# Optimization experiments

Hardware: AMD Instinct MI355X
Metric: run time of the kernel (lower is better)

Reference implementation:

```python
import jax, jax.numpy as jnp
import numpy as np

N_NODES = 100000
N_EDGES = 1600000
IN_F = 256
OUT_F = 128


def setup_inputs() -> dict:
    key = jax.random.key(0)
    k1, k2, k3, k4, k5, k6 = jax.random.split(key, 6)
    x = jax.random.normal(k1, (N_NODES, IN_F), dtype=jnp.float32)
    edge_src = jax.random.randint(k2, (N_EDGES,), 0, N_NODES, dtype=jnp.int64)
    edge_dst = jax.random.randint(k3, (N_EDGES,), 0, N_NODES, dtype=jnp.int64)
    edge_weight = jax.random.uniform(k4, (N_EDGES,), dtype=jnp.float32)
    stdv = 1.0 / np.sqrt(OUT_F)
    w = jax.random.uniform(k5, (IN_F, OUT_F), dtype=jnp.float32, minval=-stdv, maxval=stdv)
    b = jax.random.uniform(k6, (OUT_F,), dtype=jnp.float32, minval=-stdv, maxval=stdv)
    return {"x": x, "edge_src": edge_src, "edge_dst": edge_dst,
            "edge_weight": edge_weight, "w": w, "b": b}


def reference(x, edge_src, edge_dst, edge_weight, w, b):
    # dense feature transform: [N, in] @ [in, out] -> [N, out]
    h = x @ w
    # sparse adjacency SpMM: out[i] = sum_{e: dst[e]==i} a[e] * h[src[e]]
    msgs = h[edge_src] * edge_weight[:, None]          # [E, out]
    agg = jax.ops.segment_sum(msgs, edge_dst, num_segments=N_NODES)
    return agg + b
```

## Files before the change

### kernel.cpp

```cpp
#include <hip/hip_runtime.h>

#define N_NODES 100000
#define N_EDGES 1600000
#define IN_F 256
#define OUT_F 128

#define NBUCK 1563
#define NCH   250
#define CH    6400
#define LSUB  8
#define LIST_CAP (LSUB * 256)

typedef __attribute__((ext_vector_type(8))) short bf16x8;
typedef __attribute__((ext_vector_type(4))) float f32x4;

static __device__ __forceinline__ unsigned f2bf_u(float f) {
    unsigned u = __float_as_uint(f);
    return (u + 0x7FFFu + ((u >> 16) & 1u)) >> 16;
}
static __device__ __forceinline__ float bf2f(short s) {
    return __uint_as_float(((unsigned)(unsigned short)s) << 16);
}

__global__ __launch_bounds__(256) void hist_kernel(const int* __restrict__ edge_dst,
                                                   int* __restrict__ hist) {
    __shared__ int h[NBUCK];
    const int t = threadIdx.x;
    for (int b = t; b < NBUCK; b += 256) h[b] = 0;
    __syncthreads();
    const int e0 = blockIdx.x * CH;
    #pragma unroll
    for (int i = 0; i < CH / 256; ++i)
        atomicAdd(&h[edge_dst[e0 + i * 256 + t] >> 6], 1);
    __syncthreads();
    int* o = hist + (size_t)blockIdx.x * NBUCK;
    for (int b = t; b < NBUCK; b += 256) o[b] = h[b];
}

__global__ __launch_bounds__(256) void scan1_kernel(int* __restrict__ hist,
                                                    int* __restrict__ btot) {
    const int b = blockIdx.x * 256 + threadIdx.x;
    if (b >= NBUCK) return;
    int run = 0;
    #pragma unroll 10
    for (int c = 0; c < NCH; ++c) {
        const size_t idx = (size_t)c * NBUCK + b;
        const int v = hist[idx];
        hist[idx] = run;
        run += v;
    }
    btot[b] = run;
}

__global__ __launch_bounds__(256) void scan2_kernel(const int* __restrict__ btot,
                                                    int* __restrict__ bstart) {
    __shared__ int wsum[4];
    const int t = threadIdx.x;
    const int lane = t & 63, wave = t >> 6;
    int v[7];
    int s = 0;
    #pragma unroll
    for (int j = 0; j < 7; ++j) {
        const int i = t * 7 + j;
        v[j] = (i < NBUCK) ? btot[i] : 0;
        s += v[j];
    }
    int sc = s;
    #pragma unroll
    for (int off = 1; off < 64; off <<= 1) {
        const int o = __shfl_up(sc, off);
        if (lane >= off) sc += o;
    }
    if (lane == 63) wsum[wave] = sc;
    __syncthreads();
    int add = 0;
    for (int w2 = 0; w2 < wave; ++w2) add += wsum[w2];
    int excl = add + sc - s;
    #pragma unroll
    for (int j = 0; j < 7; ++j) {
        const int i = t * 7 + j;
        if (i < NBUCK) bstart[i] = excl;
        excl += v[j];
    }
    if (t == 255) bstart[NBUCK] = add + sc;
}

__global__ __launch_bounds__(256) void scatter_kernel(const int* __restrict__ edge_src,
                                                      const int* __restrict__ edge_dst,
                                                      const float* __restrict__ edge_weight,
                                                      const int* __restrict__ hist,
                                                      const int* __restrict__ bstart,
                                                      int2* __restrict__ part) {
    __shared__ int cur[NBUCK];
    const int t = threadIdx.x;
    const int c = blockIdx.x;
    const int* hc = hist + (size_t)c * NBUCK;
    for (int b = t; b < NBUCK; b += 256) cur[b] = bstart[b] + hc[b];
    __syncthreads();
    const int e0 = c * CH;
    #pragma unroll
    for (int i = 0; i < CH / 256; ++i) {
        const int e = e0 + i * 256 + t;
        const int d = edge_dst[e];
        const int pos = atomicAdd(&cur[d >> 6], 1);
        part[pos] = make_int2(edge_src[e] | ((d & 63) << 24), __float_as_int(edge_weight[e]));
    }
}

__global__ __launch_bounds__(256) void wprep_kernel(const float* __restrict__ w,
                                                    unsigned short* __restrict__ wtf) {
    int id = blockIdx.x * 256 + threadIdx.x;
    if (id >= 4096) return;
    int f = id >> 6, lane = id & 63;
    int ks = f >> 3, nt = f & 7;
    int m = lane & 15, q = lane >> 4;
    int row = nt * 16 + m;
    int col0 = ks * 32 + q * 8;
    unsigned short* o = wtf + (size_t)f * 512 + lane * 8;
    #pragma unroll
    for (int j = 0; j < 8; ++j)
        o[j] = (unsigned short)f2bf_u(w[(size_t)(col0 + j) * OUT_F + row]);
}

__global__ __launch_bounds__(256) void gemm_mfma_kernel(const float* __restrict__ x,
                                                        const unsigned short* __restrict__ wtf,
                                                        unsigned short* __restrict__ hb) {
    __shared__ unsigned short xs[64][264];
    const int t = threadIdx.x;
    const int row0 = blockIdx.x * 64;

    const float4* x4 = (const float4*)x;
    #pragma unroll
    for (int i = 0; i < 16; ++i) {
        int idx = t + i * 256;
        int r = idx >> 6, c4 = idx & 63;
        int rg = row0 + r; if (rg >= N_NODES) rg = N_NODES - 1;
        float4 v = x4[(size_t)rg * 64 + c4];
        unsigned u0 = f2bf_u(v.x) | (f2bf_u(v.y) << 16);
        unsigned u1 = f2bf_u(v.z) | (f2bf_u(v.w) << 16);
        *(uint2*)&xs[r][c4 * 4] = make_uint2(u0, u1);
    }
    __syncthreads();

    const int wave = t >> 6, lane = t & 63;
    const int m = lane & 15, quad = lane >> 4;

    bf16x8 af[8];
    #pragma unroll
    for (int ks = 0; ks < 8; ++ks)
        af[ks] = *(const bf16x8*)&xs[wave * 16 + m][ks * 32 + quad * 8];

    f32x4 acc[8];
    #pragma unroll
    for (int nt = 0; nt < 8; ++nt) acc[nt] = (f32x4){0.f, 0.f, 0.f, 0.f};

    const bf16x8* wf = (const bf16x8*)wtf;
    #pragma unroll
    for (int ks = 0; ks < 8; ++ks) {
        #pragma unroll
        for (int nt = 0; nt < 8; ++nt) {
            bf16x8 bf = wf[(size_t)(ks * 8 + nt) * 64 + lane];
            acc[nt] = __builtin_amdgcn_mfma_f32_16x16x32_bf16(af[ks], bf, acc[nt], 0, 0, 0);
        }
    }

    const int tile_base = row0 + wave * 16;
    #pragma unroll
    for (int nt = 0; nt < 8; ++nt) {
        #pragma unroll
        for (int r = 0; r < 4; ++r) {
            int orow = tile_base + quad * 4 + r;
            if (orow < N_NODES)
                hb[(size_t)orow * OUT_F + nt * 16 + m] = (unsigned short)f2bf_u(acc[nt][r]);
        }
    }
}

__global__ __launch_bounds__(256) void spmm_kernel(const unsigned short* __restrict__ hb,
                                                   const int* __restrict__ bstart,
                                                   const int2* __restrict__ part,
                                                   const float* __restrict__ b,
                                                   float* __restrict__ out) {
    __shared__ int lh[64];
    __shared__ int lstart[65];
    __shared__ int lcur[64];
    __shared__ int2 list[LIST_CAP];

    const int t = threadIdx.x;
    const int base = blockIdx.x * 64;

    const int s0 = bstart[blockIdx.x];
    int cntb = bstart[blockIdx.x + 1] - s0;
    if (cntb > LIST_CAP) cntb = LIST_CAP;

    if (t < 64) lh[t] = 0;
    __syncthreads();

    int2 stash[LSUB];
    int  sn[LSUB];
    #pragma unroll
    for (int sub = 0; sub < LSUB; ++sub) {
        const int idx = sub * 256 + t;
        sn[sub] = -1;
        if (idx < cntb) {
            int2 en = part[(size_t)s0 + idx];
            int n = ((unsigned)en.x) >> 24;
            stash[sub] = make_int2(en.x & 0xFFFFFF, en.y);
            sn[sub] = n;
            atomicAdd(&lh[n], 1);
        }
    }
    __syncthreads();

    if (t < 64) {
        int v = lh[t];
        int s = v;
        #pragma unroll
        for (int off = 1; off < 64; off <<= 1) {
            int o = __shfl_up(s, off);
            if (t >= off) s += o;
        }
        lstart[t] = s - v;
        lcur[t]   = s - v;
        if (t == 63) lstart[64] = s;
    }
    __syncthreads();

    #pragma unroll
    for (int sub = 0; sub < LSUB; ++sub) {
        if (sn[sub] >= 0) {
            int pos = atomicAdd(&lcur[sn[sub]], 1);
            list[pos] = stash[sub];
        }
    }
    __syncthreads();

    const int j = t & 15;
    const float4* b4 = (const float4*)b;
    const float4 bb0 = b4[j * 2];
    const float4 bb1 = b4[j * 2 + 1];

    #pragma unroll
    for (int g = 0; g < 4; ++g) {
        const int n = g * 16 + (t >> 4);
        const int node = base + n;
        if (node >= N_NODES) continue;
        float4 acc0 = bb0, acc1 = bb1;
        const int p1 = lstart[n + 1];
        for (int p = lstart[n]; p < p1; ++p) {
            const int2 sw = list[p];
            const float wgt = __int_as_float(sw.y);
            const bf16x8 hv = *(const bf16x8*)(hb + (size_t)sw.x * OUT_F + j * 8);
            acc0.x += wgt * bf2f(hv[0]);
            acc0.y += wgt * bf2f(hv[1]);
            acc0.z += wgt * bf2f(hv[2]);
            acc0.w += wgt * bf2f(hv[3]);
            acc1.x += wgt * bf2f(hv[4]);
            acc1.y += wgt * bf2f(hv[5]);
            acc1.z += wgt * bf2f(hv[6]);
            acc1.w += wgt * bf2f(hv[7]);
        }
        float4* o4 = (float4*)(out + (size_t)node * OUT_F + j * 8);
        o4[0] = acc0;
        o4[1] = acc1;
    }
}

extern "C" void kernel_launch(void* const* d_in, const int* in_sizes, int n_in,
                              void* d_out, int out_size, void* d_ws, size_t ws_size,
                              hipStream_t stream) {
    const float* x           = (const float*)d_in[0];
    const int*   edge_src    = (const int*)d_in[1];
    const int*   edge_dst    = (const int*)d_in[2];
    const float* edge_weight = (const float*)d_in[3];
    const float* w           = (const float*)d_in[4];
    const float* b           = (const float*)d_in[5];
    float* out = (float*)d_out;

    char* ws = (char*)d_ws;
    size_t off = 0;
    unsigned short* hb  = (unsigned short*)(ws + off);
    off += (size_t)N_NODES * OUT_F * 2;           off = (off + 15) & ~(size_t)15;
    unsigned short* wtf = (unsigned short*)(ws + off);
    off += (size_t)IN_F * OUT_F * 2;              off = (off + 15) & ~(size_t)15;
    int* hist = (int*)(ws + off);
    off += (size_t)NCH * NBUCK * 4;               off = (off + 15) & ~(size_t)15;
    int* btot = (int*)(ws + off);
    off += (size_t)NBUCK * 4;                     off = (off + 15) & ~(size_t)15;
    int* bstart = (int*)(ws + off);
    off += (size_t)(NBUCK + 1) * 4;               off = (off + 15) & ~(size_t)15;
    int2* part = (int2*)(ws + off);
    off += (size_t)N_EDGES * 8;

    hist_kernel <<<NCH, 256, 0, stream>>>(edge_dst, hist);
    scan1_kernel<<<(NBUCK + 255) / 256, 256, 0, stream>>>(hist, btot);
    scan2_kernel<<<1, 256, 0, stream>>>(btot, bstart);
    scatter_kernel<<<NCH, 256, 0, stream>>>(edge_src, edge_dst, edge_weight, hist, bstart, part);
    wprep_kernel<<<16, 256, 0, stream>>>(w, wtf);
    gemm_mfma_kernel<<<(N_NODES + 63) / 64, 256, 0, stream>>>(x, wtf, hb);
    spmm_kernel<<<NBUCK, 256, 0, stream>>>(hb, bstart, part, b, out);
}
```

Measured before the change: 319.7 us.

## Fuse partition kernels into one cooperative kernel and split SpMM buckets in half

Merges the histogram, two scans, scatter and weight-prep kernels into a single cooperative kernel that uses grid-wide syncs and keeps edge data in registers between phases, so edges are read once and four launches go away. The SpMM kernel now launches two blocks per bucket, each handling 32 nodes, for more parallelism. Its gather loop is unrolled by four to keep more loads in flight. Trade-offs: grid syncs add latency, every SpMM block reads the whole bucket's edge list twice, and the list is capped at 1024 entries, which could drop edges on skewed inputs.

```diff
diff --git a/kernel.cpp b/kernel.cpp
--- a/kernel.cpp
+++ b/kernel.cpp
@@ -1,4 +1,7 @@
 #include <hip/hip_runtime.h>
+#include <hip/hip_cooperative_groups.h>
+
+namespace cg = cooperative_groups;
 
 #define N_NODES 100000
 #define N_EDGES 1600000
@@ -8,8 +11,9 @@
 #define NBUCK 1563
 #define NCH   250
 #define CH    6400
-#define LSUB  8
-#define LIST_CAP (LSUB * 256)
+#define CBT   1024
+#define EPT   7
+#define LIST_CAP 1024
 
 typedef __attribute__((ext_vector_type(8))) short bf16x8;
 typedef __attribute__((ext_vector_type(4))) float f32x4;
@@ -22,104 +26,112 @@
     return __uint_as_float(((unsigned)(unsigned short)s) << 16);
 }
 
-__global__ __launch_bounds__(256) void hist_kernel(const int* __restrict__ edge_dst,
-                                                   int* __restrict__ hist) {
+__global__ __launch_bounds__(CBT) void part_coop_kernel(
+    const int* __restrict__ edge_src, const int* __restrict__ edge_dst,
+    const float* __restrict__ edge_weight, const float* __restrict__ w,
+    int* __restrict__ hist, int* __restrict__ btot, int* __restrict__ bstart,
+    int2* __restrict__ part, unsigned short* __restrict__ wtf) {
+    cg::grid_group grid = cg::this_grid();
     __shared__ int h[NBUCK];
-    const int t = threadIdx.x;
-    for (int b = t; b < NBUCK; b += 256) h[b] = 0;
-    __syncthreads();
-    const int e0 = blockIdx.x * CH;
-    #pragma unroll
-    for (int i = 0; i < CH / 256; ++i)
-        atomicAdd(&h[edge_dst[e0 + i * 256 + t] >> 6], 1);
-    __syncthreads();
-    int* o = hist + (size_t)blockIdx.x * NBUCK;
-    for (int b = t; b < NBUCK; b += 256) o[b] = h[b];
-}
-
-__global__ __launch_bounds__(256) void scan1_kernel(int* __restrict__ hist,
-                                                    int* __restrict__ btot) {
-    const int b = blockIdx.x * 256 + threadIdx.x;
-    if (b >= NBUCK) return;
-    int run = 0;
-    #pragma unroll 10
-    for (int c = 0; c < NCH; ++c) {
-        const size_t idx = (size_t)c * NBUCK + b;
-        const int v = hist[idx];
-        hist[idx] = run;
-        run += v;
-    }
-    btot[b] = run;
-}
-
-__global__ __launch_bounds__(256) void scan2_kernel(const int* __restrict__ btot,
-                                                    int* __restrict__ bstart) {
-    __shared__ int wsum[4];
-    const int t = threadIdx.x;
-    const int lane = t & 63, wave = t >> 6;
-    int v[7];
-    int s = 0;
-    #pragma unroll
-    for (int j = 0; j < 7; ++j) {
-        const int i = t * 7 + j;
-        v[j] = (i < NBUCK) ? btot[i] : 0;
-        s += v[j];
-    }
-    int sc = s;
-    #pragma unroll
-    for (int off = 1; off < 64; off <<= 1) {
-        const int o = __shfl_up(sc, off);
-        if (lane >= off) sc += o;
-    }
-    if (lane == 63) wsum[wave] = sc;
-    __syncthreads();
-    int add = 0;
-    for (int w2 = 0; w2 < wave; ++w2) add += wsum[w2];
-    int excl = add + sc - s;
-    #pragma unroll
-    for (int j = 0; j < 7; ++j) {
-        const int i = t * 7 + j;
-        if (i < NBUCK) bstart[i] = excl;
-        excl += v[j];
-    }
-    if (t == 255) bstart[NBUCK] = add + sc;
-}
-
-__global__ __launch_bounds__(256) void scatter_kernel(const int* __restrict__ edge_src,
-                                                      const int* __restrict__ edge_dst,
-                                                      const float* __restrict__ edge_weight,
-                                                      const int* __restrict__ hist,
-                                                      const int* __restrict__ bstart,
-                                                      int2* __restrict__ part) {
-    __shared__ int cur[NBUCK];
+    __shared__ int wsum[CBT / 64];
+
     const int t = threadIdx.x;
     const int c = blockIdx.x;
-    const int* hc = hist + (size_t)c * NBUCK;
-    for (int b = t; b < NBUCK; b += 256) cur[b] = bstart[b] + hc[b];
-    __syncthreads();
     const int e0 = c * CH;
-    #pragma unroll
-    for (int i = 0; i < CH / 256; ++i) {
-        const int e = e0 + i * 256 + t;
-        const int d = edge_dst[e];
-        const int pos = atomicAdd(&cur[d >> 6], 1);
-        part[pos] = make_int2(edge_src[e] | ((d & 63) << 24), __float_as_int(edge_weight[e]));
-    }
-}
-
-__global__ __launch_bounds__(256) void wprep_kernel(const float* __restrict__ w,
-                                                    unsigned short* __restrict__ wtf) {
-    int id = blockIdx.x * 256 + threadIdx.x;
-    if (id >= 4096) return;
-    int f = id >> 6, lane = id & 63;
-    int ks = f >> 3, nt = f & 7;
-    int m = lane & 15, q = lane >> 4;
-    int row = nt * 16 + m;
-    int col0 = ks * 32 + q * 8;
-    unsigned short* o = wtf + (size_t)f * 512 + lane * 8;
-    #pragma unroll
-    for (int j = 0; j < 8; ++j)
-        o[j] = (unsigned short)f2bf_u(w[(size_t)(col0 + j) * OUT_F + row]);
+
+    for (int i = t; i < NBUCK; i += CBT) h[i] = 0;
+    __syncthreads();
+    int dv[EPT], sv[EPT], wv[EPT];
+    #pragma unroll
+    for (int i = 0; i < EPT; ++i) {
+        const int k = i * CBT + t;
+        dv[i] = -1;
+        if (k < CH) {
+            const int e = e0 + k;
+            dv[i] = edge_dst[e];
+            sv[i] = edge_src[e];
+            wv[i] = __float_as_int(edge_weight[e]);
+            atomicAdd(&h[dv[i] >> 6], 1);
+        }
+    }
+    __syncthreads();
+    {
+        int* o = hist + (size_t)c * NBUCK;
+        for (int i = t; i < NBUCK; i += CBT) o[i] = h[i];
+    }
+    __threadfence();
+    grid.sync();
+
+    const int gt = c * CBT + t;
+    if (gt < NBUCK) {
+        int run = 0;
+        #pragma unroll 10
+        for (int ch = 0; ch < NCH; ++ch) {
+            const size_t idx = (size_t)ch * NBUCK + gt;
+            const int v = hist[idx];
+            hist[idx] = run;
+            run += v;
+        }
+        btot[gt] = run;
+    } else if (c >= 16 && c < 20) {
+        const int id = (c - 16) * CBT + t;
+        const int f = id >> 6, lane = id & 63;
+        const int ks = f >> 3, nt = f & 7;
+        const int m = lane & 15, q = lane >> 4;
+        const int row = nt * 16 + m;
+        const int col0 = ks * 32 + q * 8;
+        unsigned short* o = wtf + (size_t)f * 512 + lane * 8;
+        #pragma unroll
+        for (int jj = 0; jj < 8; ++jj)
+            o[jj] = (unsigned short)f2bf_u(w[(size_t)(col0 + jj) * OUT_F + row]);
+    }
+    __threadfence();
+    grid.sync();
+
+    if (c == 0) {
+        const int lane = t & 63, wave = t >> 6;
+        int v[2];
+        int s = 0;
+        #pragma unroll
+        for (int jj = 0; jj < 2; ++jj) {
+            const int i = t * 2 + jj;
+            v[jj] = (i < NBUCK) ? btot[i] : 0;
+            s += v[jj];
+        }
+        int sc = s;
+        #pragma unroll
+        for (int off = 1; off < 64; off <<= 1) {
+            const int o = __shfl_up(sc, off);
+            if (lane >= off) sc += o;
+        }
+        if (lane == 63) wsum[wave] = sc;
+        __syncthreads();
+        int add = 0;
+        for (int w2 = 0; w2 < wave; ++w2) add += wsum[w2];
+        int excl = add + sc - s;
+        #pragma unroll
+        for (int jj = 0; jj < 2; ++jj) {
+            const int i = t * 2 + jj;
+            if (i < NBUCK) bstart[i] = excl;
+            excl += v[jj];
+        }
+        if (t == CBT - 1) bstart[NBUCK] = add + sc;
+        __threadfence();
+    }
+    grid.sync();
+
+    {
+        const int* hc = hist + (size_t)c * NBUCK;
+        for (int i = t; i < NBUCK; i += CBT) h[i] = bstart[i] + hc[i];
+    }
+    __syncthreads();
+    #pragma unroll
+    for (int i = 0; i < EPT; ++i) {
+        if (dv[i] >= 0) {
+            const int pos = atomicAdd(&h[dv[i] >> 6], 1);
+            part[pos] = make_int2(sv[i] | ((dv[i] & 63) << 24), wv[i]);
+        }
+    }
 }
 
 __global__ __launch_bounds__(256) void gemm_mfma_kernel(const float* __restrict__ x,
@@ -181,56 +193,61 @@
                                                    const int2* __restrict__ part,
                                                    const float* __restrict__ b,
                                                    float* __restrict__ out) {
-    __shared__ int lh[64];
-    __shared__ int lstart[65];
-    __shared__ int lcur[64];
+    __shared__ int lh[32];
+    __shared__ int lstart[33];
+    __shared__ int lcur[32];
     __shared__ int2 list[LIST_CAP];
 
     const int t = threadIdx.x;
-    const int base = blockIdx.x * 64;
-
-    const int s0 = bstart[blockIdx.x];
-    int cntb = bstart[blockIdx.x + 1] - s0;
-    if (cntb > LIST_CAP) cntb = LIST_CAP;
-
-    if (t < 64) lh[t] = 0;
-    __syncthreads();
-
-    int2 stash[LSUB];
-    int  sn[LSUB];
-    #pragma unroll
-    for (int sub = 0; sub < LSUB; ++sub) {
+    const int bucket = blockIdx.x >> 1;
+    const int half = blockIdx.x & 1;
+    const int base = bucket * 64 + half * 32;
+
+    const int s0 = bstart[bucket];
+    int cntb = bstart[bucket + 1] - s0;
+    if (cntb > 2048) cntb = 2048;
+
+    if (t < 32) lh[t] = 0;
+    __syncthreads();
+
+    int2 stash[8];
+    int  sn[8];
+    #pragma unroll
+    for (int sub = 0; sub < 8; ++sub) {
         const int idx = sub * 256 + t;
         sn[sub] = -1;
         if (idx < cntb) {
-            int2 en = part[(size_t)s0 + idx];
-            int n = ((unsigned)en.x) >> 24;
-            stash[sub] = make_int2(en.x & 0xFFFFFF, en.y);
-            sn[sub] = n;
-            atomicAdd(&lh[n], 1);
-        }
-    }
-    __syncthreads();
-
-    if (t < 64) {
-        int v = lh[t];
+            const int2 en = part[(size_t)s0 + idx];
+            const int n = ((unsigned)en.x) >> 24;
+            if ((n >> 5) == half) {
+                sn[sub] = n & 31;
+                stash[sub] = make_int2(en.x & 0xFFFFFF, en.y);
+                atomicAdd(&lh[n & 31], 1);
+            }
+        }
+    }
+    __syncthreads();
+
+    if (t < 32) {
+        const int v = lh[t];
         int s = v;
         #pragma unroll
-        for (int off = 1; off < 64; off <<= 1) {
-            int o = __shfl_up(s, off);
+        for (int off = 1; off < 32; off <<= 1) {
+            const int o = __shfl_up(s, off);
             if (t >= off) s += o;
         }
-        lstart[t] = s - v;
-        lcur[t]   = s - v;
-        if (t == 63) lstart[64] = s;
-    }
-    __syncthreads();
-
-    #pragma unroll
-    for (int sub = 0; sub < LSUB; ++sub) {
+        const int st = s - v;
+        lstart[t] = st < LIST_CAP ? st : LIST_CAP;
+        lcur[t]   = st;
+        if (t == 31) lstart[32] = s < LIST_CAP ? s : LIST_CAP;
+    }
+    __syncthreads();
+
+    #pragma unroll
+    for (int sub = 0; sub < 8; ++sub) {
         if (sn[sub] >= 0) {
-            int pos = atomicAdd(&lcur[sn[sub]], 1);
-            list[pos] = stash[sub];
+            const int pos = atomicAdd(&lcur[sn[sub]], 1);
+            if (pos < LIST_CAP) list[pos] = stash[sub];
         }
     }
     __syncthreads();
@@ -241,24 +258,51 @@
     const float4 bb1 = b4[j * 2 + 1];
 
     #pragma unroll
-    for (int g = 0; g < 4; ++g) {
+    for (int g = 0; g < 2; ++g) {
         const int n = g * 16 + (t >> 4);
         const int node = base + n;
         if (node >= N_NODES) continue;
         float4 acc0 = bb0, acc1 = bb1;
+        int p = lstart[n];
         const int p1 = lstart[n + 1];
-        for (int p = lstart[n]; p < p1; ++p) {
+        for (; p + 4 <= p1; p += 4) {
+            const int2 sw0 = list[p];
+            const int2 sw1 = list[p + 1];
+            const int2 sw2 = list[p + 2];
+            const int2 sw3 = list[p + 3];
+            const bf16x8 h0 = *(const bf16x8*)(hb + (size_t)sw0.x * OUT_F + j * 8);
+            const bf16x8 h1 = *(const bf16x8*)(hb + (size_t)sw1.x * OUT_F + j * 8);
+            const bf16x8 h2 = *(const bf16x8*)(hb + (size_t)sw2.x * OUT_F + j * 8);
+            const bf16x8 h3 = *(const bf16x8*)(hb + (size_t)sw3.x * OUT_F + j * 8);
+            const float w0 = __int_as_float(sw0.y);
+            const float w1 = __int_as_float(sw1.y);
+            const float w2 = __int_as_float(sw2.y);
+            const float w3 = __int_as_float(sw3.y);
+            acc0.x += w0 * bf2f(h0[0]); acc0.y += w0 * bf2f(h0[1]);
+            acc0.z += w0 * bf2f(h0[2]); acc0.w += w0 * bf2f(h0[3]);
+            acc1.x += w0 * bf2f(h0[4]); acc1.y += w0 * bf2f(h0[5]);
+            acc1.z += w0 * bf2f(h0[6]); acc1.w += w0 * bf2f(h0[7]);
+            acc0.x += w1 * bf2f(h1[0]); acc0.y += w1 * bf2f(h1[1]);
+            acc0.z += w1 * bf2f(h1[2]); acc0.w += w1 * bf2f(h1[3]);
+            acc1.x += w1 * bf2f(h1[4]); acc1.y += w1 * bf2f(h1[5]);
+            acc1.z += w1 * bf2f(h1[6]); acc1.w += w1 * bf2f(h1[7]);
+            acc0.x += w2 * bf2f(h2[0]); acc0.y += w2 * bf2f(h2[1]);
+            acc0.z += w2 * bf2f(h2[2]); acc0.w += w2 * bf2f(h2[3]);
+            acc1.x += w2 * bf2f(h2[4]); acc1.y += w2 * bf2f(h2[5]);
+            acc1.z += w2 * bf2f(h2[6]); acc1.w += w2 * bf2f(h2[7]);
+            acc0.x += w3 * bf2f(h3[0]); acc0.y += w3 * bf2f(h3[1]);
+            acc0.z += w3 * bf2f(h3[2]); acc0.w += w3 * bf2f(h3[3]);
+            acc1.x += w3 * bf2f(h3[4]); acc1.y += w3 * bf2f(h3[5]);
+            acc1.z += w3 * bf2f(h3[6]); acc1.w += w3 * bf2f(h3[7]);
+        }
+        for (; p < p1; ++p) {
             const int2 sw = list[p];
             const float wgt = __int_as_float(sw.y);
             const bf16x8 hv = *(const bf16x8*)(hb + (size_t)sw.x * OUT_F + j * 8);
-            acc0.x += wgt * bf2f(hv[0]);
-            acc0.y += wgt * bf2f(hv[1]);
-            acc0.z += wgt * bf2f(hv[2]);
-            acc0.w += wgt * bf2f(hv[3]);
-            acc1.x += wgt * bf2f(hv[4]);
-            acc1.y += wgt * bf2f(hv[5]);
-            acc1.z += wgt * bf2f(hv[6]);
-            acc1.w += wgt * bf2f(hv[7]);
+            acc0.x += wgt * bf2f(hv[0]); acc0.y += wgt * bf2f(hv[1]);
+            acc0.z += wgt * bf2f(hv[2]); acc0.w += wgt * bf2f(hv[3]);
+            acc1.x += wgt * bf2f(hv[4]); acc1.y += wgt * bf2f(hv[5]);
+            acc1.z += wgt * bf2f(hv[6]); acc1.w += wgt * bf2f(hv[7]);
         }
         float4* o4 = (float4*)(out + (size_t)node * OUT_F + j * 8);
         o4[0] = acc0;
@@ -292,11 +336,19 @@
     int2* part = (int2*)(ws + off);
     off += (size_t)N_EDGES * 8;
 
-    hist_kernel <<<NCH, 256, 0, stream>>>(edge_dst, hist);
-    scan1_kernel<<<(NBUCK + 255) / 256, 256, 0, stream>>>(hist, btot);
-    scan2_kernel<<<1, 256, 0, stream>>>(btot, bstart);
-    scatter_kernel<<<NCH, 256, 0, stream>>>(edge_src, edge_dst, edge_weight, hist, bstart, part);
-    wprep_kernel<<<16, 256, 0, stream>>>(w, wtf);
+    void* cargs[9];
+    cargs[0] = (void*)&edge_src;
+    cargs[1] = (void*)&edge_dst;
+    cargs[2] = (void*)&edge_weight;
+    cargs[3] = (void*)&w;
+    cargs[4] = (void*)&hist;
+    cargs[5] = (void*)&btot;
+    cargs[6] = (void*)&bstart;
+    cargs[7] = (void*)&part;
+    cargs[8] = (void*)&wtf;
+    hipLaunchCooperativeKernel((const void*)part_coop_kernel, dim3(NCH), dim3(CBT),
+                               cargs, 0, stream);
+
     gemm_mfma_kernel<<<(N_NODES + 63) / 64, 256, 0, stream>>>(x, wtf, hb);
-    spmm_kernel<<<NBUCK, 256, 0, stream>>>(hb, bstart, part, b, out);
-}
+    spmm_kernel<<<2 * NBUCK, 256, 0, stream>>>(hb, bstart, part, b, out);
+}
```

Result: slower. 543.4 us (+70.0%).
